# Performance work log

Hardware: AMD Instinct MI355X
Metric: run time of the kernel (lower is better)

Reference implementation:

```python
import jax, jax.numpy as jnp
import numpy as np

RES = 0.03
NUM_ROTS = 36
NUM_PROPOSAL = 256
OVERSAMPLE = 4           # fixed-size stand-in for the data-dependent while loop
GX, GY, GZ = 272, 112, 272  # grid covering [-4,4.16] x [-0.2,3.16] x [-4,4.16] at res=0.03
POW = 0.5
SEED_DIST_THRESH = 0.3


def setup_inputs() -> dict:
    key = jax.random.key(0)
    ks = jax.random.split(key, 6)
    N, M = 100000, 1024
    extent = jnp.array([7.0, 3.0, 7.0], jnp.float32)
    offset = jnp.array([-3.5, 0.0, -3.5], jnp.float32)
    pc = jax.random.uniform(ks[0], (N, 3), jnp.float32) * extent + offset
    xyz = jax.random.uniform(ks[1], (N, 3), jnp.float32, minval=-0.3, maxval=0.3)
    scale = jax.random.uniform(ks[2], (N, 3), jnp.float32, minval=0.1, maxval=1.0)
    prob = jax.random.uniform(ks[3], (N,), jnp.float32)
    corners = jnp.array([[-4.0, -0.2, -4.0], [4.16, 3.16, 4.16]], jnp.float32)
    vote_points = jax.random.uniform(ks[4], (M, 3), jnp.float32) * extent + offset
    return dict(pc=pc, xyz=xyz, scale=scale, prob=prob, corners=corners, vote_points=vote_points)


def hough_vote(pc, xyz, scale, prob, corners):
    # Each point casts NUM_ROTS votes: center = pc + R_y(theta) @ xyz_offset
    thetas = 2.0 * jnp.pi * jnp.arange(NUM_ROTS, dtype=jnp.float32) / NUM_ROTS
    c, s = jnp.cos(thetas), jnp.sin(thetas)  # [R]
    ox, oy, oz = xyz[:, 0:1], xyz[:, 1:2], xyz[:, 2:3]  # [N,1]
    rx = ox * c + oz * s      # [N,R]
    rz = -ox * s + oz * c     # [N,R]
    tx = pc[:, 0:1] + rx
    ty = jnp.broadcast_to(pc[:, 1:2] + oy, tx.shape)
    tz = pc[:, 2:3] + rz
    ix = jnp.floor((tx - corners[0, 0]) / RES + 0.5).astype(jnp.int32)
    iy = jnp.floor((ty - corners[0, 1]) / RES + 0.5).astype(jnp.int32)
    iz = jnp.floor((tz - corners[0, 2]) / RES + 0.5).astype(jnp.int32)
    inb = ((ix >= 0) & (ix < GX) & (iy >= 0) & (iy < GY) & (iz >= 0) & (iz < GZ))
    ixc = jnp.clip(ix, 0, GX - 1)
    iyc = jnp.clip(iy, 0, GY - 1)
    izc = jnp.clip(iz, 0, GZ - 1)
    flat = ((ixc * GY + iyc) * GZ + izc).ravel()  # [N*R]
    w = (prob[:, None] * inb.astype(prob.dtype))  # [N,R]
    grid_obj = jnp.zeros((GX * GY * GZ,), pc.dtype).at[flat].add(w.ravel())
    ws = (w[:, :, None] * scale[:, None, :]).reshape(-1, 3)
    grid_scale = jnp.zeros((GX * GY * GZ, 3), pc.dtype).at[flat].add(ws)
    hv_map = grid_obj.reshape(GX, GY, GZ)
    hv_scale = (grid_scale / (grid_obj[:, None] + 1e-7)).reshape(GX, GY, GZ, 3)
    return hv_map, hv_scale


def reference(pc, xyz, scale, prob, corners, vote_points):
    hv_map, hv_scale = hough_vote(pc, xyz, scale, prob, corners)
    hv_map_y = jnp.power(hv_map.max(axis=1) + 1e-7, POW)  # [GX,GZ]
    hv_map_yidx = jnp.argmax(hv_map, axis=1)              # [GX,GZ]
    dist = hv_map_y.reshape(-1)
    finite = jnp.isfinite(dist)
    safe = jnp.where(finite, dist, 0.0)
    ok = finite.all() & (safe.sum() >= 1e-7)
    dist = jnp.where(ok, safe, 1.0)

    # fixed-size oversampling instead of the data-dependent while loop
    K = NUM_PROPOSAL * OVERSAMPLE
    sample = jax.random.categorical(jax.random.key(42), jnp.log(dist + 1e-30), shape=(K,))
    sample_val = dist[sample]
    xi = sample // GZ
    zi = sample % GZ
    yi = hv_map_yidx[xi, zi]
    world_loc = jnp.stack([xi, yi, zi], -1).astype(pc.dtype) * RES + corners[0]  # [K,3]
    sc = hv_scale[xi, yi, zi, :]  # [K,3]

    # min distance to vote seeds; keep candidates near seeds (fallback: keep all)
    d2seed = jnp.min(jnp.linalg.norm(world_loc[:, None, :] - vote_points[None, :, :], axis=-1), axis=-1)
    keep = d2seed < SEED_DIST_THRESH
    keep = jnp.where(keep.any(), keep, jnp.ones_like(keep))
    order = jnp.argsort(jnp.where(keep, 0, 1))  # stable: passing candidates first
    sel = order[:NUM_PROPOSAL]
    candidates = world_loc[sel]
    scales_out = sc[sel]
    probs = jnp.zeros((NUM_PROPOSAL,), pc.dtype)
    return candidates, probs, scales_out
```

## Files before the change

### kernel.cpp

```cpp
#include <hip/hip_runtime.h>
#include <math.h>
#include <stdio.h>
#include <stdint.h>

#define GXD 272
#define GYD 112
#define GZD 272
#define NROT 36
#define CCLS (GXD*GZD)
#define CBLK (CCLS/256)
#define KSMP 1024
#define NPROP 256
#define HSLOTS 2048
#define YH 56
#define NBINS (GXD*2)
#define SLICE (GYD*GZD)
#define SVCAP 96
#define AROWS 32
#define AUNITS (CBLK * (KSMP/AROWS))
#define TH_SPEC 0xFFE00000u

struct RotTab { float c[NROT]; float s[NROT]; };

__device__ __forceinline__ uint32_t cell_hash(int flat) {
    return ((uint32_t)flat * 2654435761u) >> 21;
}

#define ROTL_AB(x, r) __builtin_amdgcn_alignbit((x), (x), 32u - (r))

__device__ __forceinline__ uint32_t tf_bits(uint32_t i) {
    constexpr uint32_t K1  = 42u;
    constexpr uint32_t KS2 = 42u ^ 0x1BD11BDAu;
    uint32_t x0 = 0u, x1 = i + K1;
#define TF_R(r)  { x0 += x1; x1 = ROTL_AB(x1, r); x1 ^= x0; }
#define TF_RI(r, I0, I1) { x1 += (I1); x0 = x0 + (I0) + x1; x1 = ROTL_AB(x1, r); x1 ^= x0; }
    TF_R(13) TF_R(15) TF_R(26) TF_R(6)
    TF_RI(17, K1,  KS2 + 1u)  TF_R(29) TF_R(16) TF_R(24)
    TF_RI(13, KS2, 2u)        TF_R(15) TF_R(26) TF_R(6)
    TF_RI(17, 0u,  K1 + 3u)   TF_R(29) TF_R(16) TF_R(24)
    TF_RI(13, K1,  KS2 + 4u)  TF_R(15) TF_R(26) TF_R(6)
#undef TF_R
#undef TF_RI
    return (x0 + KS2) ^ (x1 + 5u);
}

__device__ __forceinline__ float uniform_from_bits(uint32_t b) {
    const float TINY = 1.1754943508222875e-38f;
    float f = __uint_as_float((b >> 9) | 0x3f800000u) - 1.0f;
    float u = __fadd_rn(__fmul_rn(f, 1.0f), TINY);
    return fmaxf(TINY, u);
}

__device__ __forceinline__ float gumbel_from_u(float u) {
    float l1 = (float)log((double)u);
    float l2 = (float)log((double)(-l1));
    return -l2;
}

__device__ __forceinline__ void phaseA_unit(int unit, int* __restrict__ svcnt,
                                            uint2* __restrict__ svrec) {
    int cb = unit % CBLK;
    int rg = unit / CBLK;
    int c  = cb * 256 + threadIdx.x;
    int k0 = rg * AROWS;
    uint32_t i = (uint32_t)k0 * (uint32_t)CCLS + (uint32_t)c;
#pragma unroll 4
    for (int kk = 0; kk < AROWS; ++kk) {
        uint32_t bits = tf_bits(i);
        if (__builtin_expect(bits >= TH_SPEC, 0)) {
            int row = k0 + kk;
            int idx = atomicAdd(&svcnt[row], 1);
            if (idx < SVCAP) svrec[row * SVCAP + idx] = make_uint2((uint32_t)c, bits);
        }
        i += (uint32_t)CCLS;
    }
}

__device__ __forceinline__ bool vote_iy(float py, float oy, float c0y, int& iy) {
    float ty = __fadd_rn(py, oy);
    float vy = __fadd_rn(__fdiv_rn(__fsub_rn(ty, c0y), 0.03f), 0.5f);
    iy = (int)floorf(vy);
    return (iy >= 0 && iy < GYD);
}
__device__ __forceinline__ bool vote_xz(float px, float pz, float ox, float oz,
                                        float c, float s, float c0x, float c0z,
                                        int& ix, int& iz) {
    float rx = __fadd_rn(__fmul_rn(ox, c), __fmul_rn(oz, s));
    float rz = __fadd_rn(__fmul_rn(-ox, s), __fmul_rn(oz, c));
    float tx = __fadd_rn(px, rx);
    float tz = __fadd_rn(pz, rz);
    float vx = __fadd_rn(__fdiv_rn(__fsub_rn(tx, c0x), 0.03f), 0.5f);
    float vz = __fadd_rn(__fdiv_rn(__fsub_rn(tz, c0z), 0.03f), 0.5f);
    ix = (int)floorf(vx);
    iz = (int)floorf(vz);
    return (ix >= 0 && ix < GXD && iz >= 0 && iz < GZD);
}

__global__ __launch_bounds__(256) void k_count_b(const float* __restrict__ pc, const float* __restrict__ xyz,
                          const float* __restrict__ corners, int N, RotTab rt,
                          int* __restrict__ bincnt, int* __restrict__ hblk,
                          int nOrig, int unitBase, int* __restrict__ svcnt, uint2* __restrict__ svrec) {
    if ((int)blockIdx.x >= nOrig) { phaseA_unit(unitBase + (int)blockIdx.x - nOrig, svcnt, svrec); return; }
    __shared__ int h[NBINS];
    int tid = threadIdx.x;
    for (int j = tid; j < NBINS; j += 256) h[j] = 0;
    __syncthreads();
    int i = blockIdx.x * 256 + tid;
    if (i < N) {
        float px = pc[3*i], py = pc[3*i+1], pz = pc[3*i+2];
        float ox = xyz[3*i], oy = xyz[3*i+1], oz = xyz[3*i+2];
        int iy;
        if (vote_iy(py, oy, corners[1], iy)) {
            int ybit = (iy >= YH) ? 1 : 0;
            float c0x = corners[0], c0z = corners[2];
            for (int r = 0; r < NROT; ++r) {
                int ix, iz;
                if (vote_xz(px, pz, ox, oz, rt.c[r], rt.s[r], c0x, c0z, ix, iz))
                    atomicAdd(&h[ix*2 + ybit], 1);
            }
        }
    }
    __syncthreads();
    int* hb = hblk + (size_t)blockIdx.x * NBINS;
    for (int j = tid; j < NBINS; j += 256) {
        int cnt = h[j];
        hb[j] = cnt;
        if (cnt) atomicAdd(&bincnt[j], cnt);
    }
}

__global__ __launch_bounds__(576) void k_prefix(const int* __restrict__ bincnt,
                         int* __restrict__ binbase, int* __restrict__ bincur) {
    __shared__ int sc[576];
    int tid = threadIdx.x;
    int v = (tid < NBINS) ? bincnt[tid] : 0;
    sc[tid] = v;
    __syncthreads();
    for (int off = 1; off < 576; off <<= 1) {
        int x = sc[tid];
        if (tid >= off) x += sc[tid - off];
        __syncthreads();
        sc[tid] = x;
        __syncthreads();
    }
    if (tid < NBINS) {
        int excl = sc[tid] - v;
        binbase[tid] = excl;
        bincur[tid] = excl;
    }
}

__global__ __launch_bounds__(256) void k_binwrite_b(const float* __restrict__ pc, const float* __restrict__ xyz,
                          const float* __restrict__ prob, const float* __restrict__ corners,
                          int N, RotTab rt, int* __restrict__ bincur,
                          const int* __restrict__ hblk, uint2* __restrict__ vrec,
                          int nOrig, int unitBase, int* __restrict__ svcnt, uint2* __restrict__ svrec) {
    if ((int)blockIdx.x >= nOrig) { phaseA_unit(unitBase + (int)blockIdx.x - nOrig, svcnt, svrec); return; }
    __shared__ int h[NBINS];
    __shared__ int bbase[NBINS];
    int tid = threadIdx.x;
    const int* hb = hblk + (size_t)blockIdx.x * NBINS;
    for (int j = tid; j < NBINS; j += 256) {
        int cnt = hb[j];
        bbase[j] = cnt ? atomicAdd(&bincur[j], cnt) : 0;
        h[j] = 0;
    }
    __syncthreads();
    int i = blockIdx.x * 256 + tid;
    if (i < N) {
        float px = pc[3*i], py = pc[3*i+1], pz = pc[3*i+2];
        float ox = xyz[3*i], oy = xyz[3*i+1], oz = xyz[3*i+2];
        int iy;
        if (vote_iy(py, oy, corners[1], iy)) {
            int ybit = (iy >= YH) ? 1 : 0;
            float c0x = corners[0], c0z = corners[2];
            float w0 = prob[i];
            for (int r = 0; r < NROT; ++r) {
                int ix, iz;
                if (vote_xz(px, pz, ox, oz, rt.c[r], rt.s[r], c0x, c0z, ix, iz)) {
                    int bin = ix*2 + ybit;
                    int rank = atomicAdd(&h[bin], 1);
                    int slot = bbase[bin] + rank;
                    vrec[slot] = make_uint2((uint32_t)((ix*GYD + iy)*GZD + iz), __float_as_uint(w0));
                }
            }
        }
    }
}

__global__ __launch_bounds__(256) void k_accum(const int* __restrict__ binbase,
                          const int* __restrict__ bincnt,
                          const uint2* __restrict__ vrec,
                          float* __restrict__ gobj,
                          unsigned long long* __restrict__ packed) {
    __shared__ float tile[YH*GZD];
    int b = blockIdx.x;
    int x = b >> 1, yh = b & 1;
    int tid = threadIdx.x;
    for (int j = tid; j < YH*GZD; j += 256) tile[j] = 0.0f;
    __syncthreads();
    int lo = binbase[b], n = bincnt[b];
    int xoff = x * SLICE;
    int yoff = yh * (YH*GZD);
    int sub = xoff + yoff;
    for (int j = lo + tid; j < lo + n; j += 256) {
        uint2 rec = vrec[j];
        atomicAdd(&tile[(int)rec.x - sub], __uint_as_float(rec.y));
    }
    __syncthreads();
    float* dst = gobj + (size_t)sub;
    for (int j = tid; j < YH*GZD; j += 256) dst[j] = tile[j];
    int ybase = yh * YH;
    for (int z = tid; z < GZD; z += 256) {
        float m = tile[z];
        int mi = 0;
        for (int y = 1; y < YH; ++y) {
            float v = tile[y*GZD + z];
            if (v > m) { m = v; mi = y; }
        }
        unsigned long long key = ((unsigned long long)__float_as_uint(m) << 32)
                               | (unsigned long long)(uint32_t)(0x7F - (ybase + mi));
        atomicMax(&packed[x*GZD + z], key);
    }
}

__global__ __launch_bounds__(256) void k_colmax2_b(const unsigned long long* __restrict__ packed,
                         float* __restrict__ logits, int* __restrict__ yidx,
                         float* __restrict__ sumdist,
                         int nOrig, int unitBase, int* __restrict__ svcnt, uint2* __restrict__ svrec) {
    if ((int)blockIdx.x >= nOrig) { phaseA_unit(unitBase + (int)blockIdx.x - nOrig, svcnt, svrec); return; }
    int c = blockIdx.x * 256 + threadIdx.x;
    unsigned long long key = packed[c];
    float m = __uint_as_float((uint32_t)(key >> 32));
    int mi = 0x7F - (int)(uint32_t)(key & 0xFFFFFFFFu);
    float d = __fsqrt_rn(__fadd_rn(m, 1e-7f));
    yidx[c] = mi;
    logits[c] = (float)log((double)__fadd_rn(d, 1e-30f));
    __shared__ float sred[256];
    int tid = threadIdx.x;
    sred[tid] = d; __syncthreads();
    for (int off = 128; off > 0; off >>= 1) {
        if (tid < off) sred[tid] += sred[tid+off];
        __syncthreads();
    }
    if (tid == 0) atomicAdd(sumdist, sred[0]);
}

__global__ __launch_bounds__(256) void k_hotthresh_b(const float* __restrict__ logits,
                                                     const float* __restrict__ sumdist,
                                                     uint32_t* __restrict__ bth,
                                                     int* __restrict__ hotcnt, int* __restrict__ hotlist,
                                                     int nOrig, int unitBase,
                                                     int* __restrict__ svcnt, uint2* __restrict__ svrec) {
    if ((int)blockIdx.x >= nOrig) { phaseA_unit(unitBase + (int)blockIdx.x - nOrig, svcnt, svrec); return; }
    int c = blockIdx.x * 256 + threadIdx.x;
    double B0 = log((double)*sumdist) - 3.0;
    double t = exp(-exp((double)logits[c] - (B0 - 0.05)));
    long long k_th = (long long)floor(t * 8388608.0) - 2;
    uint32_t b;
    if (k_th <= 0)              b = 0u;
    else if (k_th >= 8388608LL) b = 0xFFFFFFFFu;
    else                        b = (uint32_t)k_th << 9;
    bth[c] = b;
    if (b < TH_SPEC) {
        int idx = atomicAdd(hotcnt, 1);
        hotlist[idx] = c;
    }
}

__global__ __launch_bounds__(256) void k_phaseB(const uint32_t* __restrict__ bth,
                                                const int* __restrict__ hotlist,
                                                const int* __restrict__ hotcnt,
                                                int* __restrict__ svcnt, uint2* __restrict__ svrec) {
    int k = blockIdx.x;
    int n = *hotcnt;
    uint32_t base = (uint32_t)k * (uint32_t)CCLS;
    for (int j = threadIdx.x; j < n; j += 256) {
        int c = hotlist[j];
        uint32_t bits = tf_bits(base + (uint32_t)c);
        if (bits >= bth[c] && bits < TH_SPEC) {
            int idx = atomicAdd(&svcnt[k], 1);
            if (idx < SVCAP) svrec[k * SVCAP + idx] = make_uint2((uint32_t)c, bits);
        }
    }
}

__global__ __launch_bounds__(64) void k_finalize(const float* __restrict__ logits,
                                                 const float* __restrict__ sumdist,
                                                 const int* __restrict__ svcnt,
                                                 const uint2* __restrict__ svrec,
                                                 const int* __restrict__ yidx,
                                                 int* __restrict__ hkeys,
                                                 int* __restrict__ samples) {
    int k = blockIdx.x;
    int tid = threadIdx.x;
    int n = svcnt[k];
    float best = -INFINITY; int bc = 0x7fffffff;
    bool full = (n <= 0 || n > SVCAP);
    if (!full) {
        for (int j = tid; j < n; j += 64) {
            uint2 rec = svrec[k * SVCAP + j];
            int c = (int)rec.x;
            float v = __fadd_rn(gumbel_from_u(uniform_from_bits(rec.y)), logits[c]);
            if (v > best || (v == best && c < bc)) { best = v; bc = c; }
        }
        for (int off = 32; off > 0; off >>= 1) {
            float v2 = __shfl_xor(best, off);
            int   i2 = __shfl_xor(bc, off);
            if (v2 > best || (v2 == best && i2 < bc)) { best = v2; bc = i2; }
        }
        double B0 = log((double)*sumdist) - 3.0;
        if (!((double)best > B0 - 0.05)) full = true;
    }
    if (full) {
        best = -INFINITY; bc = 0x7fffffff;
        uint32_t base = (uint32_t)k * (uint32_t)CCLS;
        for (int c = tid; c < CCLS; c += 64) {
            float v = __fadd_rn(gumbel_from_u(uniform_from_bits(tf_bits(base + (uint32_t)c))), logits[c]);
            if (v > best || (v == best && c < bc)) { best = v; bc = c; }
        }
        for (int off = 32; off > 0; off >>= 1) {
            float v2 = __shfl_xor(best, off);
            int   i2 = __shfl_xor(bc, off);
            if (v2 > best || (v2 == best && i2 < bc)) { best = v2; bc = i2; }
        }
    }
    if (tid == 0) {
        samples[k] = bc;
        int xi = bc / GZD, zi = bc % GZD;
        int yi = yidx[bc];
        int flat = (xi*GYD + yi)*GZD + zi;
        uint32_t h = cell_hash(flat);
        for (;;) {
            int prev = atomicCAS(&hkeys[h], -1, flat);
            if (prev == -1 || prev == flat) break;
            h = (h + 1) & (HSLOTS - 1);
        }
    }
}

__global__ __launch_bounds__(256) void k_scale_scatter(const float* __restrict__ pc, const float* __restrict__ xyz,
                          const float* __restrict__ scale, const float* __restrict__ prob,
                          const float* __restrict__ corners,
                          const int* __restrict__ hkeys, float* __restrict__ gsmall,
                          int N, RotTab rt) {
    __shared__ int lk[HSLOTS];
    for (int j = threadIdx.x; j < HSLOTS; j += 256) lk[j] = hkeys[j];
    __syncthreads();
    int i = blockIdx.x * 256 + threadIdx.x;
    if (i >= N) return;
    float px = pc[3*i], py = pc[3*i+1], pz = pc[3*i+2];
    float ox = xyz[3*i], oy = xyz[3*i+1], oz = xyz[3*i+2];
    int iy;
    if (!vote_iy(py, oy, corners[1], iy)) return;
    float c0x = corners[0], c0z = corners[2];
    int iyo = iy * GZD;
    float w0 = prob[i];
    float ws0 = __fmul_rn(w0, scale[3*i]);
    float ws1 = __fmul_rn(w0, scale[3*i+1]);
    float ws2 = __fmul_rn(w0, scale[3*i+2]);
    for (int r = 0; r < NROT; ++r) {
        int ix, iz;
        if (!vote_xz(px, pz, ox, oz, rt.c[r], rt.s[r], c0x, c0z, ix, iz)) continue;
        int flat = ix * SLICE + iyo + iz;
        uint32_t h = cell_hash(flat);
        int slot = -1;
        for (;;) {
            int key = lk[h];
            if (key == flat) { slot = (int)h; break; }
            if (key == -1) break;
            h = (h + 1) & (HSLOTS - 1);
        }
        if (slot < 0) continue;
        atomicAdd(&gsmall[3*slot+0], ws0);
        atomicAdd(&gsmall[3*slot+1], ws1);
        atomicAdd(&gsmall[3*slot+2], ws2);
    }
}

__global__ __launch_bounds__(256) void k_post(const float* __restrict__ gobj,
                       const int* __restrict__ hkeys, const float* __restrict__ gsmall,
                       const int* __restrict__ yidx, const int* __restrict__ samples,
                       const float* __restrict__ corners, const float* __restrict__ vp, int M,
                       float* __restrict__ world, float* __restrict__ scv, int* __restrict__ keep) {
    int k = blockIdx.x;
    int tid = threadIdx.x;
    int s = samples[k];
    int xi = s / GZD, zi = s % GZD;
    int yi = yidx[s];
    float wx = __fadd_rn(__fmul_rn((float)xi, 0.03f), corners[0]);
    float wy = __fadd_rn(__fmul_rn((float)yi, 0.03f), corners[1]);
    float wz = __fadd_rn(__fmul_rn((float)zi, 0.03f), corners[2]);

    float dmin = INFINITY;
    for (int j = tid; j < M; j += 256) {
        float dx = __fsub_rn(wx, vp[3*j]);
        float dy = __fsub_rn(wy, vp[3*j+1]);
        float dz = __fsub_rn(wz, vp[3*j+2]);
        float sq = __fadd_rn(__fadd_rn(__fmul_rn(dx,dx), __fmul_rn(dy,dy)), __fmul_rn(dz,dz));
        dmin = fminf(dmin, __fsqrt_rn(sq));
    }
    __shared__ float sm[256];
    sm[tid] = dmin; __syncthreads();
    for (int off = 128; off > 0; off >>= 1) {
        if (tid < off) sm[tid] = fminf(sm[tid], sm[tid+off]);
        __syncthreads();
    }
    if (tid == 0) {
        world[3*k] = wx; world[3*k+1] = wy; world[3*k+2] = wz;
        int flat = (xi*GYD + yi)*GZD + zi;
        uint32_t h = cell_hash(flat);
        while (hkeys[h] != flat) h = (h + 1) & (HSLOTS - 1);
        float go = __fadd_rn(gobj[flat], 1e-7f);
        scv[3*k+0] = __fdiv_rn(gsmall[3*h+0], go);
        scv[3*k+1] = __fdiv_rn(gsmall[3*h+1], go);
        scv[3*k+2] = __fdiv_rn(gsmall[3*h+2], go);
        keep[k] = (sm[0] < 0.3f) ? 1 : 0;
    }
}

__global__ __launch_bounds__(256) void k_select(const float* __restrict__ world,
                                                const float* __restrict__ scv,
                                                const int* __restrict__ keep,
                                                float* __restrict__ out) {
    __shared__ int kp[KSMP];
    __shared__ int tsum[256];
    __shared__ int sel[NPROP];
    __shared__ int anyk;
    int tid = threadIdx.x;
    if (tid == 0) anyk = 0;
    __syncthreads();
    int a = 0;
    for (int j = tid; j < KSMP; j += 256) { int v = keep[j]; kp[j] = v; a |= v; }
    if (a) anyk = 1;
    __syncthreads();
    int any = anyk;
    int j0 = tid * 4;
    int k0v = any ? kp[j0]   : 1;
    int k1v = any ? kp[j0+1] : 1;
    int k2v = any ? kp[j0+2] : 1;
    int k3v = any ? kp[j0+3] : 1;
    int s0 = k0v, s1 = s0 + k1v, s2 = s1 + k2v, s3 = s2 + k3v;
    tsum[tid] = s3;
    __syncthreads();
    for (int off = 1; off < 256; off <<= 1) {
        int x = tsum[tid];
        if (tid >= off) x += tsum[tid - off];
        __syncthreads();
        tsum[tid] = x;
        __syncthreads();
    }
    int base = (tid > 0) ? tsum[tid-1] : 0;
    int nk = tsum[255];
    int inc[4] = { base + s0, base + s1, base + s2, base + s3 };
    int kv[4]  = { k0v, k1v, k2v, k3v };
    for (int q = 0; q < 4; ++q) {
        int j = j0 + q;
        int slot = kv[q] ? (inc[q] - 1) : (nk + j - inc[q]);
        if (slot < NPROP) sel[slot] = j;
    }
    __syncthreads();
    if (tid < NPROP) {
        int sidx = sel[tid];
        out[3*tid+0] = world[3*sidx+0];
        out[3*tid+1] = world[3*sidx+1];
        out[3*tid+2] = world[3*sidx+2];
        out[3*NPROP + tid] = 0.0f;
        out[4*NPROP + 3*tid + 0] = scv[3*sidx+0];
        out[4*NPROP + 3*tid + 1] = scv[3*sidx+1];
        out[4*NPROP + 3*tid + 2] = scv[3*sidx+2];
    }
}

extern "C" void kernel_launch(void* const* d_in, const int* in_sizes, int n_in,
                              void* d_out, int out_size, void* d_ws, size_t ws_size,
                              hipStream_t stream) {
    const float* pc      = (const float*)d_in[0];
    const float* xyz     = (const float*)d_in[1];
    const float* scale   = (const float*)d_in[2];
    const float* prob    = (const float*)d_in[3];
    const float* corners = (const float*)d_in[4];
    const float* vp      = (const float*)d_in[5];
    int N = in_sizes[0] / 3;
    int M = in_sizes[5] / 3;
    int NV = N * NROT;
    int pblocks = (N + 255) / 256;

    const size_t G = (size_t)GXD * GYD * GZD;
    float* gobj    = (float*)d_ws;
    float* sumdist = gobj + G;
    int*   bincnt  = (int*)(sumdist + 1);
    int*   svcnt   = bincnt + NBINS;
    int*   hotcnt  = svcnt + KSMP;
    unsigned long long* packed = (unsigned long long*)(hotcnt + 1);
    float* gsmall  = (float*)(packed + CCLS);
    size_t zero_bytes = (size_t)((char*)(gsmall + 3*HSLOTS) - (char*)sumdist);
    int*   binbase = (int*)(gsmall + 3*HSLOTS);
    int*   bincur  = binbase + NBINS;
    float* logits  = (float*)(bincur + NBINS);
    uint32_t* bth  = (uint32_t*)(logits + CCLS);
    int*   yidx    = (int*)(bth + CCLS);
    int*   samples = yidx + CCLS;
    int*   hkeys   = samples + KSMP;
    float* world   = (float*)(hkeys + HSLOTS);
    float* scv     = world + 3*KSMP;
    int*   keep    = (int*)(scv + 3*KSMP);
    uint2* svrec   = (uint2*)(((uintptr_t)(keep + KSMP) + 15) & ~(uintptr_t)15);
    int*   hotlist = (int*)(svrec + (size_t)KSMP * SVCAP);
    int*   hblk    = hotlist + CCLS;
    uint2* vrec    = (uint2*)(((uintptr_t)(hblk + (size_t)pblocks*NBINS) + 15) & ~(uintptr_t)15);
    size_t need = (size_t)((char*)(vrec + NV) - (char*)d_ws);
    if (ws_size < need) {
        fprintf(stderr, "kernel_launch: ws_size %zu < needed %zu\n", ws_size, need);
        return;
    }

    hipMemsetAsync(sumdist, 0, zero_bytes, stream);
    hipMemsetAsync(hkeys, 0xFF, HSLOTS*sizeof(int), stream);

    RotTab rt;
    const float twopi = (float)(2.0 * M_PI);
    for (int r = 0; r < NROT; ++r) {
        float th = (twopi * (float)r) / 36.0f;
        rt.c[r] = (float)cos((double)th);
        rt.s[r] = (float)sin((double)th);
    }

    const int BAL1 = 2800, BAL2 = 2800, BAL3 = 1900, BAL4 = AUNITS - BAL1 - BAL2 - BAL3;

    k_count_b<<<pblocks + BAL1, 256, 0, stream>>>(pc, xyz, corners, N, rt, bincnt, hblk,
                                                  pblocks, 0, svcnt, svrec);
    k_prefix<<<1, 576, 0, stream>>>(bincnt, binbase, bincur);
    k_binwrite_b<<<pblocks + BAL2, 256, 0, stream>>>(pc, xyz, prob, corners, N, rt, bincur, hblk, vrec,
                                                     pblocks, BAL1, svcnt, svrec);
    k_accum<<<NBINS, 256, 0, stream>>>(binbase, bincnt, vrec, gobj, packed);
    k_colmax2_b<<<CBLK + BAL3, 256, 0, stream>>>(packed, logits, yidx, sumdist,
                                                 CBLK, BAL1 + BAL2, svcnt, svrec);
    k_hotthresh_b<<<CBLK + BAL4, 256, 0, stream>>>(logits, sumdist, bth, hotcnt, hotlist,
                                                   CBLK, BAL1 + BAL2 + BAL3, svcnt, svrec);
    k_phaseB<<<KSMP, 256, 0, stream>>>(bth, hotlist, hotcnt, svcnt, svrec);
    k_finalize<<<KSMP, 64, 0, stream>>>(logits, sumdist, svcnt, svrec, yidx, hkeys, samples);
    k_scale_scatter<<<pblocks, 256, 0, stream>>>(pc, xyz, scale, prob, corners, hkeys, gsmall, N, rt);
    k_post<<<KSMP, 256, 0, stream>>>(gobj, hkeys, gsmall, yidx, samples, corners, vp, M, world, scv, keep);
    k_select<<<1, 256, 0, stream>>>(world, scv, keep, (float*)d_out);
}
```

Measured before the change: 369.1 us.

## Pack vote records to 32 bits and drop full dense grid writeback

Vote records shrink from 8 bytes (flat cell index plus weight) to 4 bytes: a point index and a local tile offset, with the weight gathered from prob inside the accumulation kernel. The accumulation kernel no longer writes the full dense object grid to global memory. The post kernel instead reads the column max value from the packed max array, since the sampled cell is always the argmax cell. This cuts scatter and gather traffic and about 33MB of grid writes, at the cost of a random prob gather and an N limit of 2^17 imposed by the packing.

```diff
diff --git a/kernel.cpp b/kernel.cpp
--- a/kernel.cpp
+++ b/kernel.cpp
@@ -151,9 +151,9 @@
 }
 
 __global__ __launch_bounds__(256) void k_binwrite_b(const float* __restrict__ pc, const float* __restrict__ xyz,
-                          const float* __restrict__ prob, const float* __restrict__ corners,
+                          const float* __restrict__ corners,
                           int N, RotTab rt, int* __restrict__ bincur,
-                          const int* __restrict__ hblk, uint2* __restrict__ vrec,
+                          const int* __restrict__ hblk, uint32_t* __restrict__ vrec,
                           int nOrig, int unitBase, int* __restrict__ svcnt, uint2* __restrict__ svrec) {
     if ((int)blockIdx.x >= nOrig) { phaseA_unit(unitBase + (int)blockIdx.x - nOrig, svcnt, svrec); return; }
     __shared__ int h[NBINS];
@@ -173,15 +173,15 @@
         int iy;
         if (vote_iy(py, oy, corners[1], iy)) {
             int ybit = (iy >= YH) ? 1 : 0;
+            int iyrel = iy - ybit*YH;
             float c0x = corners[0], c0z = corners[2];
-            float w0 = prob[i];
             for (int r = 0; r < NROT; ++r) {
                 int ix, iz;
                 if (vote_xz(px, pz, ox, oz, rt.c[r], rt.s[r], c0x, c0z, ix, iz)) {
                     int bin = ix*2 + ybit;
                     int rank = atomicAdd(&h[bin], 1);
                     int slot = bbase[bin] + rank;
-                    vrec[slot] = make_uint2((uint32_t)((ix*GYD + iy)*GZD + iz), __float_as_uint(w0));
+                    vrec[slot] = ((uint32_t)i << 14) | (uint32_t)(iyrel*GZD + iz);
                 }
             }
         }
@@ -190,8 +190,8 @@
 
 __global__ __launch_bounds__(256) void k_accum(const int* __restrict__ binbase,
                           const int* __restrict__ bincnt,
-                          const uint2* __restrict__ vrec,
-                          float* __restrict__ gobj,
+                          const uint32_t* __restrict__ vrec,
+                          const float* __restrict__ prob,
                           unsigned long long* __restrict__ packed) {
     __shared__ float tile[YH*GZD];
     int b = blockIdx.x;
@@ -200,16 +200,11 @@
     for (int j = tid; j < YH*GZD; j += 256) tile[j] = 0.0f;
     __syncthreads();
     int lo = binbase[b], n = bincnt[b];
-    int xoff = x * SLICE;
-    int yoff = yh * (YH*GZD);
-    int sub = xoff + yoff;
     for (int j = lo + tid; j < lo + n; j += 256) {
-        uint2 rec = vrec[j];
-        atomicAdd(&tile[(int)rec.x - sub], __uint_as_float(rec.y));
-    }
-    __syncthreads();
-    float* dst = gobj + (size_t)sub;
-    for (int j = tid; j < YH*GZD; j += 256) dst[j] = tile[j];
+        uint32_t rec = vrec[j];
+        atomicAdd(&tile[rec & 0x3FFFu], prob[rec >> 14]);
+    }
+    __syncthreads();
     int ybase = yh * YH;
     for (int z = tid; z < GZD; z += 256) {
         float m = tile[z];
@@ -378,7 +373,7 @@
     }
 }
 
-__global__ __launch_bounds__(256) void k_post(const float* __restrict__ gobj,
+__global__ __launch_bounds__(256) void k_post(const unsigned long long* __restrict__ packed,
                        const int* __restrict__ hkeys, const float* __restrict__ gsmall,
                        const int* __restrict__ yidx, const int* __restrict__ samples,
                        const float* __restrict__ corners, const float* __restrict__ vp, int M,
@@ -411,7 +406,8 @@
         int flat = (xi*GYD + yi)*GZD + zi;
         uint32_t h = cell_hash(flat);
         while (hkeys[h] != flat) h = (h + 1) & (HSLOTS - 1);
-        float go = __fadd_rn(gobj[flat], 1e-7f);
+        float m = __uint_as_float((uint32_t)(packed[s] >> 32));
+        float go = __fadd_rn(m, 1e-7f);
         scv[3*k+0] = __fdiv_rn(gsmall[3*h+0], go);
         scv[3*k+1] = __fdiv_rn(gsmall[3*h+1], go);
         scv[3*k+2] = __fdiv_rn(gsmall[3*h+2], go);
@@ -485,10 +481,12 @@
     int M = in_sizes[5] / 3;
     int NV = N * NROT;
     int pblocks = (N + 255) / 256;
-
-    const size_t G = (size_t)GXD * GYD * GZD;
-    float* gobj    = (float*)d_ws;
-    float* sumdist = gobj + G;
+    if (N > (1 << 17)) {
+        fprintf(stderr, "kernel_launch: N %d exceeds packing limit\n", N);
+        return;
+    }
+
+    float* sumdist = (float*)d_ws;
     int*   bincnt  = (int*)(sumdist + 1);
     int*   svcnt   = bincnt + NBINS;
     int*   hotcnt  = svcnt + KSMP;
@@ -508,7 +506,7 @@
     uint2* svrec   = (uint2*)(((uintptr_t)(keep + KSMP) + 15) & ~(uintptr_t)15);
     int*   hotlist = (int*)(svrec + (size_t)KSMP * SVCAP);
     int*   hblk    = hotlist + CCLS;
-    uint2* vrec    = (uint2*)(((uintptr_t)(hblk + (size_t)pblocks*NBINS) + 15) & ~(uintptr_t)15);
+    uint32_t* vrec = (uint32_t*)(((uintptr_t)(hblk + (size_t)pblocks*NBINS) + 15) & ~(uintptr_t)15);
     size_t need = (size_t)((char*)(vrec + NV) - (char*)d_ws);
     if (ws_size < need) {
         fprintf(stderr, "kernel_launch: ws_size %zu < needed %zu\n", ws_size, need);
@@ -531,9 +529,9 @@
     k_count_b<<<pblocks + BAL1, 256, 0, stream>>>(pc, xyz, corners, N, rt, bincnt, hblk,
                                                   pblocks, 0, svcnt, svrec);
     k_prefix<<<1, 576, 0, stream>>>(bincnt, binbase, bincur);
-    k_binwrite_b<<<pblocks + BAL2, 256, 0, stream>>>(pc, xyz, prob, corners, N, rt, bincur, hblk, vrec,
+    k_binwrite_b<<<pblocks + BAL2, 256, 0, stream>>>(pc, xyz, corners, N, rt, bincur, hblk, vrec,
                                                      pblocks, BAL1, svcnt, svrec);
-    k_accum<<<NBINS, 256, 0, stream>>>(binbase, bincnt, vrec, gobj, packed);
+    k_accum<<<NBINS, 256, 0, stream>>>(binbase, bincnt, vrec, prob, packed);
     k_colmax2_b<<<CBLK + BAL3, 256, 0, stream>>>(packed, logits, yidx, sumdist,
                                                  CBLK, BAL1 + BAL2, svcnt, svrec);
     k_hotthresh_b<<<CBLK + BAL4, 256, 0, stream>>>(logits, sumdist, bth, hotcnt, hotlist,
@@ -541,6 +539,6 @@
     k_phaseB<<<KSMP, 256, 0, stream>>>(bth, hotlist, hotcnt, svcnt, svrec);
     k_finalize<<<KSMP, 64, 0, stream>>>(logits, sumdist, svcnt, svrec, yidx, hkeys, samples);
     k_scale_scatter<<<pblocks, 256, 0, stream>>>(pc, xyz, scale, prob, corners, hkeys, gsmall, N, rt);
-    k_post<<<KSMP, 256, 0, stream>>>(gobj, hkeys, gsmall, yidx, samples, corners, vp, M, world, scv, keep);
+    k_post<<<KSMP, 256, 0, stream>>>(packed, hkeys, gsmall, yidx, samples, corners, vp, M, world, scv, keep);
     k_select<<<1, 256, 0, stream>>>(world, scv, keep, (float*)d_out);
 }
```

Result: no change. 368.6 us (-0.1%).
